# Kernel optimization log

Measured on AMD Instinct MI355X. Metric: run time of the kernel, lower is better.

## Reference

```python
import jax, jax.numpy as jnp
import numpy as np

B, S, D, H = 2, 2048, 1024, 16
HD = D // H  # head_dim = 64


def setup_inputs() -> dict:
    key = jax.random.key(0)
    ks = jax.random.split(key, 12)
    scale = 1.0 / np.sqrt(D)
    inp = {
        "query": jax.random.normal(ks[0], (B, S, D), jnp.float32),
        "key": jax.random.normal(ks[1], (B, S, D), jnp.float32),
        "value": jax.random.normal(ks[2], (B, S, D), jnp.float32),
        # causal mask, True = masked out; shape [B, q_len, k_len]
        "mask": jnp.broadcast_to(
            jnp.triu(jnp.ones((S, S), jnp.bool_), k=1), (B, S, S)
        ),
        "Wq": jax.random.normal(ks[3], (D, D), jnp.float32) * scale,
        "bq": jnp.zeros((D,), jnp.float32),
        "Wk": jax.random.normal(ks[4], (D, D), jnp.float32) * scale,
        "bk": jnp.zeros((D,), jnp.float32),
        "Wv": jax.random.normal(ks[5], (D, D), jnp.float32) * scale,
        "bv": jnp.zeros((D,), jnp.float32),
        "Wo": jax.random.normal(ks[6], (D, D), jnp.float32) * scale,
        "bo": jnp.zeros((D,), jnp.float32),
    }
    return inp


def _split_heads(x):
    b, s, _ = x.shape
    return x.reshape(b, s, H, HD).transpose(0, 2, 1, 3)  # [B,H,S,HD]


def reference(query, key, value, mask, Wq, bq, Wk, bk, Wv, bv, Wo, bo):
    # Linear layers use torch convention: y = x @ W.T + b, W is [out, in]
    q = _split_heads(query @ Wq.T + bq)
    k = _split_heads(key @ Wk.T + bk)
    v = _split_heads(value @ Wv.T + bv)
    scores = jnp.einsum("bhqd,bhkd->bhqk", q, k) / jnp.sqrt(jnp.float32(HD))
    # normalized mask [B,1,q,k]; True means masked
    scores = jnp.where(mask[:, None, :, :], jnp.finfo(scores.dtype).min, scores)
    attn = jax.nn.softmax(scores, axis=-1)  # dropout is identity in eval
    ctx = jnp.einsum("bhqk,bhkd->bhqd", attn, v)
    merged = ctx.transpose(0, 2, 1, 3).reshape(query.shape[0], -1, D)
    out = merged @ Wo.T + bo
    return out
```

## Files before the change

### kernel.cpp

```cpp
#include <hip/hip_runtime.h>

#define B_ 2
#define S_ 2048
#define D_ 1024
#define H_ 16
#define HD_ 64
#define M_ (B_ * S_)

typedef __bf16 bf16x8 __attribute__((ext_vector_type(8)));
typedef float f32x4 __attribute__((ext_vector_type(4)));

__device__ inline unsigned short f2bf(float f) {
    unsigned int u = __builtin_bit_cast(unsigned int, f);
    u += 0x7fffu + ((u >> 16) & 1u);
    return (unsigned short)(u >> 16);
}

__device__ inline void async_ld16(const unsigned short* g, unsigned short* l) {
    __builtin_amdgcn_global_load_lds(
        (const __attribute__((address_space(1))) unsigned int*)g,
        (__attribute__((address_space(3))) unsigned int*)l, 16, 0, 0);
}

__global__ __launch_bounds__(256) void cvt_all(
    const float* __restrict__ i0, const float* __restrict__ i1, const float* __restrict__ i2,
    const float* __restrict__ i3, const float* __restrict__ i4, const float* __restrict__ i5,
    const float* __restrict__ i6,
    unsigned short* __restrict__ o0, unsigned short* __restrict__ o1, unsigned short* __restrict__ o2,
    unsigned short* __restrict__ o3, unsigned short* __restrict__ o4, unsigned short* __restrict__ o5,
    unsigned short* __restrict__ o6, int nbig, int nsmall) {
    int z = blockIdx.y;
    const float* in = (z == 0) ? i0 : (z == 1) ? i1 : (z == 2) ? i2 : (z == 3) ? i3
                     : (z == 4) ? i4 : (z == 5) ? i5 : i6;
    unsigned short* out = (z == 0) ? o0 : (z == 1) ? o1 : (z == 2) ? o2 : (z == 3) ? o3
                         : (z == 4) ? o4 : (z == 5) ? o5 : o6;
    int n = (z < 3) ? nbig : nsmall;
    int i = (blockIdx.x * 256 + threadIdx.x) * 4;
    if (i >= n) return;
    float4 v = *(const float4*)(in + i);
    ushort4 o;
    o.x = f2bf(v.x); o.y = f2bf(v.y); o.z = f2bf(v.z); o.w = f2bf(v.w);
    *(ushort4*)(out + i) = o;
}

__device__ inline void gemm_compute(const unsigned short* __restrict__ A,
                                    const unsigned short* __restrict__ W,
                                    int K, int m0, int n0,
                                    unsigned short* As0, unsigned short* As1,
                                    unsigned short* Bs0, unsigned short* Bs1,
                                    f32x4 acc[4][4]) {
    const int t = threadIdx.x;
    const int lane = t & 63, wave = t >> 6;
    const int ml = lane & 15, quad = lane >> 4;
    const int wr = (wave >> 1) * 64, wc = (wave & 1) * 64;
    const int lrow = lane >> 3;
    const int gchunk = (lane & 7) ^ lrow;

    const f32x4 zero = {0.f, 0.f, 0.f, 0.f};
    for (int i = 0; i < 4; i++)
        for (int j = 0; j < 4; j++) acc[i][j] = zero;

    const int niter = K >> 6;

    auto issue = [&](int kt, unsigned short* As, unsigned short* Bs) {
        int k0 = kt << 6;
        for (int i = 0; i < 4; i++) {
            int r = wave * 32 + i * 8;
            async_ld16(A + (size_t)(m0 + r + lrow) * K + k0 + gchunk * 8, As + r * 64);
            async_ld16(W + (size_t)(n0 + r + lrow) * K + k0 + gchunk * 8, Bs + r * 64);
        }
    };

    issue(0, As0, Bs0);
    __syncthreads();

    for (int kt = 0; kt < niter; kt++) {
        unsigned short* As = (kt & 1) ? As1 : As0;
        unsigned short* Bs = (kt & 1) ? Bs1 : Bs0;
        if (kt + 1 < niter) issue(kt + 1, (kt & 1) ? As0 : As1, (kt & 1) ? Bs0 : Bs1);

        for (int kk = 0; kk < 2; ++kk) {
            bf16x8 af[4], bfr[4];
            for (int i = 0; i < 4; i++)
                af[i] = *(const bf16x8*)(As + (wr + i * 16 + ml) * 64 + (((kk * 4 + quad) ^ (ml & 7)) << 3));
            for (int j = 0; j < 4; j++)
                bfr[j] = *(const bf16x8*)(Bs + (wc + j * 16 + ml) * 64 + (((kk * 4 + quad) ^ (ml & 7)) << 3));
            for (int i = 0; i < 4; i++)
                for (int j = 0; j < 4; j++)
                    acc[i][j] = __builtin_amdgcn_mfma_f32_16x16x32_bf16(af[i], bfr[j], acc[i][j], 0, 0, 0);
        }
        __syncthreads();
    }
}

__global__ __launch_bounds__(256) void gemm_qkv(
    const unsigned short* __restrict__ xq, const unsigned short* __restrict__ xk,
    const unsigned short* __restrict__ xv,
    const unsigned short* __restrict__ wq, const unsigned short* __restrict__ wk,
    const unsigned short* __restrict__ wv,
    const float* __restrict__ bq, const float* __restrict__ bk, const float* __restrict__ bv,
    unsigned short* __restrict__ oq, unsigned short* __restrict__ ok,
    unsigned short* __restrict__ ov) {
    extern __shared__ __align__(16) unsigned short smem[];
    unsigned short* As0 = smem;
    unsigned short* As1 = smem + 8192;
    unsigned short* Bs0 = smem + 16384;
    unsigned short* Bs1 = smem + 24576;

    const unsigned short *A, *W;
    const float* bias;
    unsigned short* out;
    int z = blockIdx.z;
    if (z == 0) { A = xq; W = wq; bias = bq; out = oq; }
    else if (z == 1) { A = xk; W = wk; bias = bk; out = ok; }
    else { A = xv; W = wv; bias = bv; out = ov; }

    int m0 = blockIdx.y * 128, n0 = blockIdx.x * 128;
    f32x4 acc[4][4];
    gemm_compute(A, W, D_, m0, n0, As0, As1, Bs0, Bs1, acc);

    const int t = threadIdx.x, lane = t & 63, wave = t >> 6;
    const int ml = lane & 15, quad = lane >> 4;
    const int wr = (wave >> 1) * 64, wc = (wave & 1) * 64;

    unsigned short* Cs = smem;
    const float sc = (z == 0) ? 0.125f : 1.0f;
    for (int i = 0; i < 4; i++)
        for (int j = 0; j < 4; j++) {
            int col = wc + j * 16 + ml;
            float bb = bias[n0 + col];
            for (int rg = 0; rg < 4; rg++) {
                int row = wr + i * 16 + quad * 4 + rg;
                unsigned short v = f2bf((acc[i][j][rg] + bb) * sc);
                if (z < 2) Cs[row * 136 + col] = v;
                else       Cs[col * 136 + row] = v;
            }
        }
    __syncthreads();

    const int r = t >> 1, hf = t & 1;
    if (z < 2) {
        unsigned short* dst = out + (size_t)(m0 + r) * D_ + n0 + hf * 64;
        const unsigned short* src = Cs + r * 136 + hf * 64;
        for (int i = 0; i < 8; i++)
            *(uint4*)(dst + i * 8) = *(const uint4*)(src + i * 8);
    } else {
        int n = n0 + r, h = n >> 6, d = n & 63;
        int b = m0 >> 11, s0 = m0 & 2047;
        unsigned short* dst = ov + ((size_t)((b * H_ + h) * 64 + d)) * S_ + s0 + hf * 64;
        const unsigned short* src = Cs + r * 136 + hf * 64;
        for (int i = 0; i < 8; i++)
            *(uint4*)(dst + i * 8) = *(const uint4*)(src + i * 8);
    }
}

__global__ __launch_bounds__(256) void gemm_out(const unsigned short* __restrict__ A,
                                                const unsigned short* __restrict__ W,
                                                const float* __restrict__ bias,
                                                float* __restrict__ out) {
    __shared__ unsigned short As0[128 * 64], As1[128 * 64], Bs0[128 * 64], Bs1[128 * 64];
    int m0 = blockIdx.y * 128, n0 = blockIdx.x * 128;
    f32x4 acc[4][4];
    gemm_compute(A, W, D_, m0, n0, As0, As1, Bs0, Bs1, acc);

    const int t = threadIdx.x, lane = t & 63, wave = t >> 6;
    const int ml = lane & 15, quad = lane >> 4;
    const int wr = (wave >> 1) * 64, wc = (wave & 1) * 64;
    for (int i = 0; i < 4; i++)
        for (int j = 0; j < 4; j++) {
            int n = n0 + wc + j * 16 + ml;
            float bb = bias[n];
            for (int rg = 0; rg < 4; rg++) {
                int m = m0 + wr + i * 16 + quad * 4 + rg;
                out[(size_t)m * D_ + n] = acc[i][j][rg] + bb;
            }
        }
}

__global__ __launch_bounds__(256, 2) void attn_kernel(const unsigned short* __restrict__ qm,
                                                      const unsigned short* __restrict__ km,
                                                      const unsigned short* __restrict__ vt,
                                                      unsigned short* __restrict__ ctx) {
    __shared__ unsigned short Ks[2][128 * 64];
    __shared__ unsigned short Vs[2][64 * 128];

    const int qb = 31 - (blockIdx.x >> 5);
    const int bh = blockIdx.x & 31;
    const int b = bh >> 4, h = bh & 15;
    const size_t vbase = (size_t)bh * S_ * 64;
    const int t = threadIdx.x, lane = t & 63, wave = t >> 6;
    const int ml = lane & 15, quad = lane >> 4;
    const int lrow = lane >> 3;
    const int gchunk = (lane & 7) ^ lrow;
    const int vrow = lane >> 4;
    const int q0 = qb * 64;

    bf16x8 qf[2];
    {
        int qrow = q0 + wave * 16 + ml;
        const unsigned short* qp = qm + (size_t)(b * S_ + qrow) * D_ + h * 64;
        qf[0] = *(const bf16x8*)(qp + quad * 8);
        qf[1] = *(const bf16x8*)(qp + 32 + quad * 8);
    }

    const f32x4 zero = {0.f, 0.f, 0.f, 0.f};
    f32x4 acc[4];
    for (int j = 0; j < 4; j++) acc[j] = zero;
    float m_i = -INFINITY, l_i = 0.f;

    const int ntiles = (qb + 2) >> 1;

    auto issue_tile = [&](int kt, int bb) {
        for (int i = 0; i < 4; i++) {
            int r = wave * 32 + i * 8;
            async_ld16(km + (size_t)(b * S_ + kt * 128 + r + lrow) * D_ + h * 64 + gchunk * 8,
                       Ks[bb] + r * 64);
            int dd = wave * 16 + i * 4;
            int d = dd + vrow;
            async_ld16(vt + vbase + (size_t)d * S_ + kt * 128 + (((lane & 15) ^ (d & 15)) << 3),
                       Vs[bb] + dd * 128);
        }
    };

    issue_tile(0, 0);
    __syncthreads();

    for (int kt = 0; kt < ntiles; kt++) {
        const int buf = kt & 1;
        if (kt + 1 < ntiles) issue_tile(kt + 1, buf ^ 1);

        f32x4 sacc[8];
        for (int n = 0; n < 8; n++) sacc[n] = zero;
        for (int n = 0; n < 8; n++)
            for (int kk = 0; kk < 2; kk++) {
                bf16x8 kf = *(const bf16x8*)(Ks[buf] + (n * 16 + ml) * 64 +
                                             (((kk * 4 + quad) ^ (ml & 7)) << 3));
                sacc[n] = __builtin_amdgcn_mfma_f32_16x16x32_bf16(kf, qf[kk], sacc[n], 0, 0, 0);
            }

        const bool last = (kt == ntiles - 1);
        const int qidx = q0 + wave * 16 + ml;
        if (last) {
            for (int n = 0; n < 8; n++)
                for (int rg = 0; rg < 4; rg++) {
                    int kidx = kt * 128 + n * 16 + quad * 4 + rg;
                    if (kidx > qidx) sacc[n][rg] = -3.0e38f;
                }
        }

        float mx = sacc[0][0];
        for (int n = 0; n < 8; n++)
            for (int rg = 0; rg < 4; rg++) mx = fmaxf(mx, sacc[n][rg]);
        mx = fmaxf(mx, __shfl_xor(mx, 16));
        mx = fmaxf(mx, __shfl_xor(mx, 32));
        float mc = fmaxf(m_i, mx);
        float al = __expf(m_i - mc);
        m_i = mc;
        float rs = 0.f;
        for (int n = 0; n < 8; n++)
            for (int rg = 0; rg < 4; rg++) {
                float p = __expf(sacc[n][rg] - mc);
                sacc[n][rg] = p;
                rs += p;
            }
        rs += __shfl_xor(rs, 16);
        rs += __shfl_xor(rs, 32);
        l_i = l_i * al + rs;

        float alT[4];
        for (int rg = 0; rg < 4; rg++) alT[rg] = __shfl(al, quad * 4 + rg);
        for (int j = 0; j < 4; j++)
            for (int rg = 0; rg < 4; rg++) acc[j][rg] *= alT[rg];

        for (int n2 = 0; n2 < 4; n2++) {
            union { bf16x8 v; unsigned short u[8]; } pk;
            for (int rg = 0; rg < 4; rg++) {
                pk.u[rg] = f2bf(sacc[2 * n2][rg]);
                pk.u[4 + rg] = f2bf(sacc[2 * n2 + 1][rg]);
            }
            const int c0 = 4 * n2 + (quad >> 1);
            const int qo = (quad & 1) << 2;
            for (int j = 0; j < 4; j++) {
                int row = j * 16 + ml;
                union { bf16x8 v; uint2 d2[2]; } vv;
                vv.d2[0] = *(const uint2*)(Vs[buf] + row * 128 + (((c0 ^ (row & 15)) << 3) + qo));
                vv.d2[1] = *(const uint2*)(Vs[buf] + row * 128 + ((((c0 + 2) ^ (row & 15)) << 3) + qo));
                acc[j] = __builtin_amdgcn_mfma_f32_16x16x32_bf16(pk.v, vv.v, acc[j], 0, 0, 0);
            }
        }

        __syncthreads();
    }

    float lT[4];
    for (int rg = 0; rg < 4; rg++) lT[rg] = __shfl(l_i, quad * 4 + rg);
    for (int j = 0; j < 4; j++) {
        int d = j * 16 + ml;
        for (int rg = 0; rg < 4; rg++) {
            int srow = q0 + wave * 16 + quad * 4 + rg;
            float val = acc[j][rg] / lT[rg];
            ctx[((size_t)(b * S_ + srow)) * D_ + h * 64 + d] = f2bf(val);
        }
    }
}

extern "C" void kernel_launch(void* const* d_in, const int* in_sizes, int n_in,
                              void* d_out, int out_size, void* d_ws, size_t ws_size,
                              hipStream_t stream) {
    const float* query = (const float*)d_in[0];
    const float* key_ = (const float*)d_in[1];
    const float* value = (const float*)d_in[2];
    const float* Wq = (const float*)d_in[4];
    const float* bq = (const float*)d_in[5];
    const float* Wk = (const float*)d_in[6];
    const float* bk = (const float*)d_in[7];
    const float* Wv = (const float*)d_in[8];
    const float* bv = (const float*)d_in[9];
    const float* Wo = (const float*)d_in[10];
    const float* bo = (const float*)d_in[11];
    float* out = (float*)d_out;

    const size_t XE = (size_t)M_ * D_;
    const size_t WE = (size_t)D_ * D_;
    char* ws = (char*)d_ws;
    unsigned short* xq = (unsigned short*)ws; ws += XE * 2;
    unsigned short* xk = (unsigned short*)ws; ws += XE * 2;
    unsigned short* xv = (unsigned short*)ws; ws += XE * 2;
    unsigned short* wqb = (unsigned short*)ws; ws += WE * 2;
    unsigned short* wkb = (unsigned short*)ws; ws += WE * 2;
    unsigned short* wvb = (unsigned short*)ws; ws += WE * 2;
    unsigned short* wob = (unsigned short*)ws; ws += WE * 2;
    unsigned short* qmb = (unsigned short*)ws; ws += XE * 2;
    unsigned short* kmb = (unsigned short*)ws; ws += XE * 2;
    unsigned short* vt = (unsigned short*)ws; ws += XE * 2;
    unsigned short* ctx = (unsigned short*)ws; ws += XE * 2;

    cvt_all<<<dim3(XE / 1024, 7), 256, 0, stream>>>(
        query, key_, value, Wq, Wk, Wv, Wo,
        xq, xk, xv, wqb, wkb, wvb, wob, (int)XE, (int)WE);

    gemm_qkv<<<dim3(D_ / 128, M_ / 128, 3), 256, 65536, stream>>>(
        xq, xk, xv, wqb, wkb, wvb, bq, bk, bv, qmb, kmb, vt);

    attn_kernel<<<dim3(1024), 256, 0, stream>>>(qmb, kmb, vt, ctx);

    gemm_out<<<dim3(D_ / 128, M_ / 128), 256, 0, stream>>>(ctx, wob, bo, out);
}
```

Measured before the change: 255.0 us.

## Process two query groups per attention block to reuse K/V tiles, remap GEMM grids

The attention kernel now handles 128 query rows per block, as two 64-row groups sharing each loaded K/V tile, so each tile feeds twice as many MFMAs. This halves the grid to 512 blocks and cuts K/V global and LDS traffic per query. It costs more registers (doubled accumulators and scores) and gives coarser causal load balance. The QKV and output GEMMs switch to a flat 1D grid with n-major block ordering, which may improve L2 reuse of the weight tiles.

```diff
diff --git a/kernel.cpp b/kernel.cpp
--- a/kernel.cpp
+++ b/kernel.cpp
@@ -14,6 +14,10 @@
     unsigned int u = __builtin_bit_cast(unsigned int, f);
     u += 0x7fffu + ((u >> 16) & 1u);
     return (unsigned short)(u >> 16);
+}
+
+__device__ inline unsigned int pk_bf16(float a, float b) {
+    return (unsigned int)f2bf(a) | ((unsigned int)f2bf(b) << 16);
 }
 
 __device__ inline void async_ld16(const unsigned short* g, unsigned short* l) {
@@ -107,15 +111,20 @@
     unsigned short* Bs0 = smem + 16384;
     unsigned short* Bs1 = smem + 24576;
 
+    const int id = blockIdx.x;
+    const int n_ = id / 96;
+    const int g = id % 96;
+    const int z = g / 32;
+    const int m_ = g % 32;
+    const int m0 = m_ * 128, n0 = n_ * 128;
+
     const unsigned short *A, *W;
     const float* bias;
     unsigned short* out;
-    int z = blockIdx.z;
     if (z == 0) { A = xq; W = wq; bias = bq; out = oq; }
     else if (z == 1) { A = xk; W = wk; bias = bk; out = ok; }
     else { A = xv; W = wv; bias = bv; out = ov; }
 
-    int m0 = blockIdx.y * 128, n0 = blockIdx.x * 128;
     f32x4 acc[4][4];
     gemm_compute(A, W, D_, m0, n0, As0, As1, Bs0, Bs1, acc);
 
@@ -159,7 +168,8 @@
                                                 const float* __restrict__ bias,
                                                 float* __restrict__ out) {
     __shared__ unsigned short As0[128 * 64], As1[128 * 64], Bs0[128 * 64], Bs1[128 * 64];
-    int m0 = blockIdx.y * 128, n0 = blockIdx.x * 128;
+    const int n_ = blockIdx.x >> 5, m_ = blockIdx.x & 31;
+    const int m0 = m_ * 128, n0 = n_ * 128;
     f32x4 acc[4][4];
     gemm_compute(A, W, D_, m0, n0, As0, As1, Bs0, Bs1, acc);
 
@@ -184,7 +194,7 @@
     __shared__ unsigned short Ks[2][128 * 64];
     __shared__ unsigned short Vs[2][64 * 128];
 
-    const int qb = 31 - (blockIdx.x >> 5);
+    const int qb = 15 - (blockIdx.x >> 5);
     const int bh = blockIdx.x & 31;
     const int b = bh >> 4, h = bh & 15;
     const size_t vbase = (size_t)bh * S_ * 64;
@@ -193,24 +203,28 @@
     const int lrow = lane >> 3;
     const int gchunk = (lane & 7) ^ lrow;
     const int vrow = lane >> 4;
-    const int q0 = qb * 64;
-
-    bf16x8 qf[2];
-    {
-        int qrow = q0 + wave * 16 + ml;
+    const int q0 = qb * 128;
+
+    bf16x8 qf[2][2];
+#pragma unroll
+    for (int g = 0; g < 2; g++) {
+        int qrow = q0 + g * 64 + wave * 16 + ml;
         const unsigned short* qp = qm + (size_t)(b * S_ + qrow) * D_ + h * 64;
-        qf[0] = *(const bf16x8*)(qp + quad * 8);
-        qf[1] = *(const bf16x8*)(qp + 32 + quad * 8);
+        qf[g][0] = *(const bf16x8*)(qp + quad * 8);
+        qf[g][1] = *(const bf16x8*)(qp + 32 + quad * 8);
     }
 
     const f32x4 zero = {0.f, 0.f, 0.f, 0.f};
-    f32x4 acc[4];
-    for (int j = 0; j < 4; j++) acc[j] = zero;
-    float m_i = -INFINITY, l_i = 0.f;
-
-    const int ntiles = (qb + 2) >> 1;
+    f32x4 acc[2][4];
+#pragma unroll
+    for (int g = 0; g < 2; g++)
+        for (int j = 0; j < 4; j++) acc[g][j] = zero;
+    float m_i[2] = {-INFINITY, -INFINITY}, l_i[2] = {0.f, 0.f};
+
+    const int ntiles = qb + 1;
 
     auto issue_tile = [&](int kt, int bb) {
+#pragma unroll
         for (int i = 0; i < 4; i++) {
             int r = wave * 32 + i * 8;
             async_ld16(km + (size_t)(b * S_ + kt * 128 + r + lrow) * D_ + h * 64 + gchunk * 8,
@@ -229,77 +243,103 @@
         const int buf = kt & 1;
         if (kt + 1 < ntiles) issue_tile(kt + 1, buf ^ 1);
 
-        f32x4 sacc[8];
-        for (int n = 0; n < 8; n++) sacc[n] = zero;
+        f32x4 sacc[2][8];
+#pragma unroll
+        for (int g = 0; g < 2; g++)
+            for (int n = 0; n < 8; n++) sacc[g][n] = zero;
+#pragma unroll
         for (int n = 0; n < 8; n++)
+#pragma unroll
             for (int kk = 0; kk < 2; kk++) {
                 bf16x8 kf = *(const bf16x8*)(Ks[buf] + (n * 16 + ml) * 64 +
                                              (((kk * 4 + quad) ^ (ml & 7)) << 3));
-                sacc[n] = __builtin_amdgcn_mfma_f32_16x16x32_bf16(kf, qf[kk], sacc[n], 0, 0, 0);
+                sacc[0][n] = __builtin_amdgcn_mfma_f32_16x16x32_bf16(kf, qf[0][kk], sacc[0][n], 0, 0, 0);
+                sacc[1][n] = __builtin_amdgcn_mfma_f32_16x16x32_bf16(kf, qf[1][kk], sacc[1][n], 0, 0, 0);
             }
 
         const bool last = (kt == ntiles - 1);
-        const int qidx = q0 + wave * 16 + ml;
-        if (last) {
+        float alv[2];
+#pragma unroll
+        for (int g = 0; g < 2; g++) {
+            if (last) {
+                const int qidx = q0 + g * 64 + wave * 16 + ml;
+#pragma unroll
+                for (int n = 0; n < 8; n++)
+                    for (int rg = 0; rg < 4; rg++) {
+                        int kidx = kt * 128 + n * 16 + quad * 4 + rg;
+                        if (kidx > qidx) sacc[g][n][rg] = -3.0e38f;
+                    }
+            }
+            float mx = sacc[g][0][0];
+#pragma unroll
+            for (int n = 0; n < 8; n++)
+                for (int rg = 0; rg < 4; rg++) mx = fmaxf(mx, sacc[g][n][rg]);
+            mx = fmaxf(mx, __shfl_xor(mx, 16));
+            mx = fmaxf(mx, __shfl_xor(mx, 32));
+            float mc = fmaxf(m_i[g], mx);
+            float al = __expf(m_i[g] - mc);
+            m_i[g] = mc;
+            float rs = 0.f;
+#pragma unroll
             for (int n = 0; n < 8; n++)
                 for (int rg = 0; rg < 4; rg++) {
-                    int kidx = kt * 128 + n * 16 + quad * 4 + rg;
-                    if (kidx > qidx) sacc[n][rg] = -3.0e38f;
+                    float p = __expf(sacc[g][n][rg] - mc);
+                    sacc[g][n][rg] = p;
+                    rs += p;
                 }
-        }
-
-        float mx = sacc[0][0];
-        for (int n = 0; n < 8; n++)
-            for (int rg = 0; rg < 4; rg++) mx = fmaxf(mx, sacc[n][rg]);
-        mx = fmaxf(mx, __shfl_xor(mx, 16));
-        mx = fmaxf(mx, __shfl_xor(mx, 32));
-        float mc = fmaxf(m_i, mx);
-        float al = __expf(m_i - mc);
-        m_i = mc;
-        float rs = 0.f;
-        for (int n = 0; n < 8; n++)
-            for (int rg = 0; rg < 4; rg++) {
-                float p = __expf(sacc[n][rg] - mc);
-                sacc[n][rg] = p;
-                rs += p;
-            }
-        rs += __shfl_xor(rs, 16);
-        rs += __shfl_xor(rs, 32);
-        l_i = l_i * al + rs;
-
-        float alT[4];
-        for (int rg = 0; rg < 4; rg++) alT[rg] = __shfl(al, quad * 4 + rg);
-        for (int j = 0; j < 4; j++)
-            for (int rg = 0; rg < 4; rg++) acc[j][rg] *= alT[rg];
-
+            rs += __shfl_xor(rs, 16);
+            rs += __shfl_xor(rs, 32);
+            l_i[g] = l_i[g] * al + rs;
+            alv[g] = al;
+        }
+#pragma unroll
+        for (int g = 0; g < 2; g++) {
+            float alT[4];
+            for (int rg = 0; rg < 4; rg++) alT[rg] = __shfl(alv[g], quad * 4 + rg);
+            for (int j = 0; j < 4; j++)
+                for (int rg = 0; rg < 4; rg++) acc[g][j][rg] *= alT[rg];
+        }
+
+#pragma unroll
         for (int n2 = 0; n2 < 4; n2++) {
-            union { bf16x8 v; unsigned short u[8]; } pk;
-            for (int rg = 0; rg < 4; rg++) {
-                pk.u[rg] = f2bf(sacc[2 * n2][rg]);
-                pk.u[4 + rg] = f2bf(sacc[2 * n2 + 1][rg]);
-            }
             const int c0 = 4 * n2 + (quad >> 1);
             const int qo = (quad & 1) << 2;
+            bf16x8 vv[4];
+#pragma unroll
             for (int j = 0; j < 4; j++) {
                 int row = j * 16 + ml;
-                union { bf16x8 v; uint2 d2[2]; } vv;
-                vv.d2[0] = *(const uint2*)(Vs[buf] + row * 128 + (((c0 ^ (row & 15)) << 3) + qo));
-                vv.d2[1] = *(const uint2*)(Vs[buf] + row * 128 + ((((c0 + 2) ^ (row & 15)) << 3) + qo));
-                acc[j] = __builtin_amdgcn_mfma_f32_16x16x32_bf16(pk.v, vv.v, acc[j], 0, 0, 0);
+                union { bf16x8 v; uint2 d2[2]; } u;
+                u.d2[0] = *(const uint2*)(Vs[buf] + row * 128 + (((c0 ^ (row & 15)) << 3) + qo));
+                u.d2[1] = *(const uint2*)(Vs[buf] + row * 128 + ((((c0 + 2) ^ (row & 15)) << 3) + qo));
+                vv[j] = u.v;
+            }
+#pragma unroll
+            for (int g = 0; g < 2; g++) {
+                union { bf16x8 v; unsigned int w[4]; } pk;
+                pk.w[0] = pk_bf16(sacc[g][2 * n2][0], sacc[g][2 * n2][1]);
+                pk.w[1] = pk_bf16(sacc[g][2 * n2][2], sacc[g][2 * n2][3]);
+                pk.w[2] = pk_bf16(sacc[g][2 * n2 + 1][0], sacc[g][2 * n2 + 1][1]);
+                pk.w[3] = pk_bf16(sacc[g][2 * n2 + 1][2], sacc[g][2 * n2 + 1][3]);
+#pragma unroll
+                for (int j = 0; j < 4; j++)
+                    acc[g][j] = __builtin_amdgcn_mfma_f32_16x16x32_bf16(pk.v, vv[j], acc[g][j], 0, 0, 0);
             }
         }
 
         __syncthreads();
     }
 
-    float lT[4];
-    for (int rg = 0; rg < 4; rg++) lT[rg] = __shfl(l_i, quad * 4 + rg);
-    for (int j = 0; j < 4; j++) {
-        int d = j * 16 + ml;
-        for (int rg = 0; rg < 4; rg++) {
-            int srow = q0 + wave * 16 + quad * 4 + rg;
-            float val = acc[j][rg] / lT[rg];
-            ctx[((size_t)(b * S_ + srow)) * D_ + h * 64 + d] = f2bf(val);
+#pragma unroll
+    for (int g = 0; g < 2; g++) {
+        float lT[4];
+        for (int rg = 0; rg < 4; rg++) lT[rg] = __shfl(l_i[g], quad * 4 + rg);
+        for (int j = 0; j < 4; j++) {
+            int d = j * 16 + ml;
+            for (int rg = 0; rg < 4; rg++) {
+                int srow = q0 + g * 64 + wave * 16 + quad * 4 + rg;
+                float val = acc[g][j][rg] / lT[rg];
+                ctx[((size_t)(b * S_ + srow)) * D_ + h * 64 + d] = f2bf(val);
+            }
         }
     }
 }
@@ -339,10 +379,10 @@
         query, key_, value, Wq, Wk, Wv, Wo,
         xq, xk, xv, wqb, wkb, wvb, wob, (int)XE, (int)WE);
 
-    gemm_qkv<<<dim3(D_ / 128, M_ / 128, 3), 256, 65536, stream>>>(
+    gemm_qkv<<<dim3(768), 256, 65536, stream>>>(
         xq, xk, xv, wqb, wkb, wvb, bq, bk, bv, qmb, kmb, vt);
 
-    attn_kernel<<<dim3(1024), 256, 0, stream>>>(qmb, kmb, vt, ctx);
-
-    gemm_out<<<dim3(D_ / 128, M_ / 128), 256, 0, stream>>>(ctx, wob, bo, out);
-}
+    attn_kernel<<<dim3(512), 256, 0, stream>>>(qmb, kmb, vt, ctx);
+
+    gemm_out<<<dim3(256), 256, 0, stream>>>(ctx, wob, bo, out);
+}
```

Measured after the change: 255.0 us. Within noise of the previous version (+0.0%).
